# Optimization experiments

Hardware: AMD Instinct MI355X
Metric: run time of the kernel (lower is better)

Reference implementation:

```python
import jax, jax.numpy as jnp
import numpy as np

N_QUBITS = 7
N_LAYERS = 2
HILBERT = 2 ** N_QUBITS


def _rx(t):
    c = jnp.cos(t / 2).astype(jnp.complex64)
    s = (-1j * jnp.sin(t / 2)).astype(jnp.complex64)
    return jnp.stack([jnp.stack([c, s]), jnp.stack([s, c])])


def _ry(t):
    c = jnp.cos(t / 2).astype(jnp.complex64)
    s = jnp.sin(t / 2).astype(jnp.complex64)
    return jnp.stack([jnp.stack([c, -s]), jnp.stack([s, c])])


def _rz(t):
    z0 = jnp.exp(-0.5j * t).astype(jnp.complex64)
    z1 = jnp.exp(0.5j * t).astype(jnp.complex64)
    zero = jnp.zeros_like(z0)
    return jnp.stack([jnp.stack([z0, zero]), jnp.stack([zero, z1])])


def _apply_1q(state, U, q):
    # state: [B, 2, 2, ..., 2]; wire q lives on axis q+1 (wire 0 = MSB, PennyLane convention)
    ax = q + 1
    out = jnp.tensordot(U, state, axes=[[1], [ax]])  # new gate axis at 0
    return jnp.moveaxis(out, 0, ax)


def _apply_cnot(state, c, t):
    c_ax, t_ax = c + 1, t + 1
    s0 = jax.lax.index_in_dim(state, 0, c_ax, keepdims=False)
    s1 = jax.lax.index_in_dim(state, 1, c_ax, keepdims=False)
    t2 = t_ax - 1 if t_ax > c_ax else t_ax  # target axis after control axis removed
    s1 = jnp.flip(s1, axis=t2)  # X on target within control=1 block
    return jnp.stack([s0, s1], axis=c_ax)


def setup_inputs() -> dict:
    key = jax.random.key(0)
    k1, k2 = jax.random.split(key)
    x = jax.random.normal(k1, (131072, HILBERT), dtype=jnp.float32)
    weights = jax.random.uniform(k2, (N_LAYERS, N_QUBITS, 3), dtype=jnp.float32) * (2 * np.pi)
    return {"x": x, "weights": weights}


def reference(x, weights):
    B = x.shape[0]
    norms = jnp.maximum(jnp.linalg.norm(x, axis=-1, keepdims=True), 1e-8)
    psi = (x / norms).astype(jnp.complex64)
    state = psi.reshape((B,) + (2,) * N_QUBITS)
    for layer in range(N_LAYERS):
        for q in range(N_QUBITS):
            state = _apply_1q(state, _rx(weights[layer, q, 0]), q)
            state = _apply_1q(state, _ry(weights[layer, q, 1]), q)
            state = _apply_1q(state, _rz(weights[layer, q, 2]), q)
        for q in range(N_QUBITS):
            state = _apply_cnot(state, q, (q + 1) % N_QUBITS)
    probs = jnp.abs(state) ** 2  # real [B, 2,...,2]
    zs = []
    for q in range(N_QUBITS):
        other = tuple(a for a in range(1, N_QUBITS + 1) if a != q + 1)
        p = probs.sum(axis=other)  # [B, 2] marginal of wire q
        zs.append(p[:, 0] - p[:, 1])
    return jnp.stack(zs, axis=-1)  # [B, N_QUBITS]
```

## Files before the change

kernel.cpp:

```cpp
#include <hip/hip_runtime.h>
#include <hip/hip_bf16.h>


typedef __attribute__((ext_vector_type(8)))  short short8;
typedef __attribute__((ext_vector_type(16))) float f32x16;

static __device__ __forceinline__ short f2bf(float f) {
  __bf16 h = (__bf16)f;
  return __builtin_bit_cast(short, h);
}

static __device__ __forceinline__ int widx(int P, int s, int k) {
  return ((((P << 2) + (s >> 5)) * 8 + (k >> 4)) * 64 +
          ((s & 31) + ((k >> 3) & 1) * 32)) * 8 + (k & 7);
}

__global__ void qnn_build_w(const float* __restrict__ wts,
                            short* __restrict__ W) {
  const int k = blockIdx.x;
  const int l = threadIdx.x;

  float c0r = (2 * l     == k) ? 1.f : 0.f, c0i = 0.f;
  float c1r = (2 * l + 1 == k) ? 1.f : 0.f, c1i = 0.f;

  for (int layer = 0; layer < 2; ++layer) {
    for (int q = 0; q < 7; ++q) {
      const float t0 = 0.5f * wts[(layer * 7 + q) * 3 + 0];
      const float t1 = 0.5f * wts[(layer * 7 + q) * 3 + 1];
      const float t2 = 0.5f * wts[(layer * 7 + q) * 3 + 2];
      const float cx = __cosf(t0), sx = __sinf(t0);
      const float cy = __cosf(t1), sy = __sinf(t1);
      const float cz = __cosf(t2), sz = __sinf(t2);
      const float m00r =  cy * cx, m00i =  sy * sx;
      const float m01r = -sy * cx, m01i = -cy * sx;
      const float m10r =  sy * cx, m10i = -cy * sx;
      const float m11r =  cy * cx, m11i = -sy * sx;
      const float g00r = m00r * cz + m00i * sz, g00i = m00i * cz - m00r * sz;
      const float g01r = m01r * cz + m01i * sz, g01i = m01i * cz - m01r * sz;
      const float g10r = m10r * cz - m10i * sz, g10i = m10i * cz + m10r * sz;
      const float g11r = m11r * cz - m11i * sz, g11i = m11i * cz + m11r * sz;

      const int b = 6 - q;
      if (b == 0) {
        const float n0r = g00r*c0r - g00i*c0i + g01r*c1r - g01i*c1i;
        const float n0i = g00r*c0i + g00i*c0r + g01r*c1i + g01i*c1r;
        const float n1r = g10r*c0r - g10i*c0i + g11r*c1r - g11i*c1i;
        const float n1i = g10r*c0i + g10i*c0r + g11r*c1i + g11i*c1r;
        c0r = n0r; c0i = n0i; c1r = n1r; c1i = n1i;
      } else {
        const int xm  = 1 << (b - 1);
        const int myb = (l >> (b - 1)) & 1;
        const float p0r = __shfl_xor(c0r, xm), p0i = __shfl_xor(c0i, xm);
        const float p1r = __shfl_xor(c1r, xm), p1i = __shfl_xor(c1i, xm);
        const float gar = myb ? g11r : g00r, gai = myb ? g11i : g00i;
        const float gbr = myb ? g10r : g01r, gbi = myb ? g10i : g01i;
        const float n0r = gar*c0r - gai*c0i + gbr*p0r - gbi*p0i;
        const float n0i = gar*c0i + gai*c0r + gbr*p0i + gbi*p0r;
        const float n1r = gar*c1r - gai*c1i + gbr*p1r - gbi*p1i;
        const float n1i = gar*c1i + gai*c1r + gbr*p1i + gbi*p1r;
        c0r = n0r; c0i = n0i; c1r = n1r; c1i = n1i;
      }
    }
    #pragma unroll
    for (int q = 0; q < 7; ++q) {
      const int bc = 6 - q;
      const int bt = 6 - ((q + 1) % 7);
      if (bt == 0) {
        if (l & 1) { float tr=c0r, ti=c0i; c0r=c1r; c0i=c1i; c1r=tr; c1i=ti; }
      } else if (bc == 0) {
        c1r = __shfl_xor(c1r, 32);
        c1i = __shfl_xor(c1i, 32);
      } else {
        const int xm = 1 << (bt - 1);
        const float p0r = __shfl_xor(c0r, xm), p0i = __shfl_xor(c0i, xm);
        const float p1r = __shfl_xor(c1r, xm), p1i = __shfl_xor(c1i, xm);
        if ((l >> (bc - 1)) & 1) { c0r=p0r; c0i=p0i; c1r=p1r; c1i=p1i; }
      }
    }
  }

  W[widx(0, 2 * l,     k)] = f2bf(c0r);
  W[widx(0, 2 * l + 1, k)] = f2bf(c1r);
  W[widx(1, 2 * l,     k)] = f2bf(c0i);
  W[widx(1, 2 * l + 1, k)] = f2bf(c1i);
}

__global__ __launch_bounds__(256, 4) void qnn_main(
    const float* __restrict__ x, const short* __restrict__ W,
    float* __restrict__ out) {
  const int tid = threadIdx.x;
  const int l   = tid & 63;
  const int wv  = tid >> 6;
  const int col = l & 31;
  const int h   = l >> 5;

  __shared__ short8 xb[512];
  __shared__ float  red[4][32][7];

  const int t0 = blockIdx.x;

  float4 fa[2], fb[2];
  #pragma unroll
  for (int i = 0; i < 2; ++i) {
    const int p = i * 256 + tid;
    const int r = p >> 4, q = p & 15;
    const float* gp = x + (size_t)(t0 * 32 + r) * 128 + q * 8;
    fa[i] = *reinterpret_cast<const float4*>(gp);
    fb[i] = *reinterpret_cast<const float4*>(gp + 4);
  }

  short8 A0[8], A1[8];
  #pragma unroll
  for (int j = 0; j < 8; ++j) {
    const int off = ((wv * 8 + j) * 64 + l) * 8;
    A0[j] = *reinterpret_cast<const short8*>(W + off);
    A1[j] = *reinterpret_cast<const short8*>(W + 16384 + off);
  }

  #pragma unroll
  for (int i = 0; i < 2; ++i) {
    const int p = i * 256 + tid;
    const int r = p >> 4, q = p & 15;
    short8 c;
    c[0]=f2bf(fa[i].x); c[1]=f2bf(fa[i].y); c[2]=f2bf(fa[i].z); c[3]=f2bf(fa[i].w);
    c[4]=f2bf(fb[i].x); c[5]=f2bf(fb[i].y); c[6]=f2bf(fb[i].z); c[7]=f2bf(fb[i].w);
    xb[r * 16 + (q ^ (r & 7))] = c;
  }
  asm volatile("s_waitcnt lgkmcnt(0)" ::: "memory");
  __builtin_amdgcn_s_barrier();
  asm volatile("" ::: "memory");

  f32x16 acc0 = {0.f,0.f,0.f,0.f,0.f,0.f,0.f,0.f,
                 0.f,0.f,0.f,0.f,0.f,0.f,0.f,0.f};
  f32x16 acc1 = {0.f,0.f,0.f,0.f,0.f,0.f,0.f,0.f,
                 0.f,0.f,0.f,0.f,0.f,0.f,0.f,0.f};
  #pragma unroll
  for (int j = 0; j < 8; ++j) {
    const int q = j * 2 + h;
    const short8 bfr = xb[col * 16 + (q ^ (col & 7))];
    acc0 = __builtin_amdgcn_mfma_f32_32x32x16_bf16(A0[j], bfr, acc0, 0, 0, 0);
    acc1 = __builtin_amdgcn_mfma_f32_32x32x16_bf16(A1[j], bfr, acc1, 0, 0, 0);
  }

  {
    float aS[8], aD[8];
    #pragma unroll
    for (int i = 0; i < 8; ++i) {
      const float pe = acc0[2*i]   * acc0[2*i]   + acc1[2*i]   * acc1[2*i];
      const float po = acc0[2*i+1] * acc0[2*i+1] + acc1[2*i+1] * acc1[2*i+1];
      aS[i] = pe + po;
      aD[i] = pe - po;
    }
    float bS[4], bD[4];
    #pragma unroll
    for (int i = 0; i < 4; ++i) {
      bS[i] = aS[2*i] + aS[2*i+1];
      bD[i] = aS[2*i] - aS[2*i+1];
    }
    float u0 = ((aD[0]+aD[1]) + (aD[2]+aD[3])) + ((aD[4]+aD[5]) + (aD[6]+aD[7]));
    float u1 = (bD[0] + bD[1]) + (bD[2] + bD[3]);
    const float cS0 = bS[0] + bS[1], cD0 = bS[0] - bS[1];
    const float cS1 = bS[2] + bS[3], cD1 = bS[2] - bS[3];
    float u3 = cD0 + cD1;
    float u4 = cS0 - cS1;
    float T  = cS0 + cS1;

    const float Tp = __shfl_xor(T, 32);
    const float u2 = h ? (Tp - T) : (T - Tp);
    T += Tp;
    u0 += __shfl_xor(u0, 32);
    u1 += __shfl_xor(u1, 32);
    u3 += __shfl_xor(u3, 32);
    u4 += __shfl_xor(u4, 32);

    if (h == 0) {
      red[wv][col][0] = T;
      red[wv][col][1] = u0;
      red[wv][col][2] = u1;
      red[wv][col][3] = u2;
      red[wv][col][4] = u3;
      red[wv][col][5] = u4;
    }
  }

  asm volatile("s_waitcnt lgkmcnt(0)" ::: "memory");
  __builtin_amdgcn_s_barrier();
  asm volatile("" ::: "memory");

  if (tid < 32) {
    const int c = tid;
    const float T0 = red[0][c][0], T1 = red[1][c][0];
    const float T2 = red[2][c][0], T3 = red[3][c][0];
    const float sT  = (T0 + T1) + (T2 + T3);
    const float inv = 1.0f / sT;
    const float z0 = (T0 + T1) - (T2 + T3);
    const float z1 = (T0 - T1) + (T2 - T3);
    float zr[5];
    #pragma unroll
    for (int i = 0; i < 5; ++i)
      zr[i] = (red[0][c][5-i] + red[1][c][5-i]) +
              (red[2][c][5-i] + red[3][c][5-i]);
    float* o = out + (size_t)(t0 * 32 + c) * 7;
    o[0] = z0 * inv; o[1] = z1 * inv; o[2] = zr[0] * inv; o[3] = zr[1] * inv;
    o[4] = zr[2] * inv; o[5] = zr[3] * inv; o[6] = zr[4] * inv;
  }
}

extern "C" void kernel_launch(void* const* d_in, const int* in_sizes, int n_in,
                              void* d_out, int out_size, void* d_ws, size_t ws_size,
                              hipStream_t stream) {
  const float* x   = (const float*)d_in[0];
  const float* wts = (const float*)d_in[1];
  float* out = (float*)d_out;
  short* W   = (short*)d_ws;

  const int B     = in_sizes[0] / 128;
  const int grid  = B / 32;

  qnn_build_w<<<128, 64, 0, stream>>>(wts, W);
  qnn_main<<<grid, 256, 0, stream>>>(x, W, out);
}
```

Before: 25.55 us.

## Make main kernel persistent with double-buffered LDS and prefetched x tiles

Changes the main kernel from one 32-row tile per block to a grid-stride persistent loop over 1024 blocks. The W fragments are loaded into registers once per block. The next tile's x is prefetched into registers and staged into a second LDS buffer while the current tile is computed. This amortises W loads and block launch overhead and overlaps global loads with MFMA work. It adds a loop, doubles the LDS buffers and keeps more registers live, which may reduce occupancy.

```diff
diff --git a/kernel.cpp b/kernel.cpp
--- a/kernel.cpp
+++ b/kernel.cpp
@@ -87,27 +87,15 @@
 
 __global__ __launch_bounds__(256, 4) void qnn_main(
     const float* __restrict__ x, const short* __restrict__ W,
-    float* __restrict__ out) {
+    float* __restrict__ out, int ntiles, int stride) {
   const int tid = threadIdx.x;
   const int l   = tid & 63;
   const int wv  = tid >> 6;
   const int col = l & 31;
   const int h   = l >> 5;
 
-  __shared__ short8 xb[512];
-  __shared__ float  red[4][32][7];
-
-  const int t0 = blockIdx.x;
-
-  float4 fa[2], fb[2];
-  #pragma unroll
-  for (int i = 0; i < 2; ++i) {
-    const int p = i * 256 + tid;
-    const int r = p >> 4, q = p & 15;
-    const float* gp = x + (size_t)(t0 * 32 + r) * 128 + q * 8;
-    fa[i] = *reinterpret_cast<const float4*>(gp);
-    fb[i] = *reinterpret_cast<const float4*>(gp + 4);
-  }
+  __shared__ short8 xb[2][512];
+  __shared__ float  red[2][4][32][6];
 
   short8 A0[8], A1[8];
   #pragma unroll
@@ -117,32 +105,40 @@
     A1[j] = *reinterpret_cast<const short8*>(W + 16384 + off);
   }
 
-  #pragma unroll
-  for (int i = 0; i < 2; ++i) {
-    const int p = i * 256 + tid;
-    const int r = p >> 4, q = p & 15;
-    short8 c;
-    c[0]=f2bf(fa[i].x); c[1]=f2bf(fa[i].y); c[2]=f2bf(fa[i].z); c[3]=f2bf(fa[i].w);
-    c[4]=f2bf(fb[i].x); c[5]=f2bf(fb[i].y); c[6]=f2bf(fb[i].z); c[7]=f2bf(fb[i].w);
-    xb[r * 16 + (q ^ (r & 7))] = c;
-  }
-  asm volatile("s_waitcnt lgkmcnt(0)" ::: "memory");
-  __builtin_amdgcn_s_barrier();
-  asm volatile("" ::: "memory");
-
-  f32x16 acc0 = {0.f,0.f,0.f,0.f,0.f,0.f,0.f,0.f,
-                 0.f,0.f,0.f,0.f,0.f,0.f,0.f,0.f};
-  f32x16 acc1 = {0.f,0.f,0.f,0.f,0.f,0.f,0.f,0.f,
-                 0.f,0.f,0.f,0.f,0.f,0.f,0.f,0.f};
-  #pragma unroll
-  for (int j = 0; j < 8; ++j) {
-    const int q = j * 2 + h;
-    const short8 bfr = xb[col * 16 + (q ^ (col & 7))];
-    acc0 = __builtin_amdgcn_mfma_f32_32x32x16_bf16(A0[j], bfr, acc0, 0, 0, 0);
-    acc1 = __builtin_amdgcn_mfma_f32_32x32x16_bf16(A1[j], bfr, acc1, 0, 0, 0);
-  }
-
-  {
+  float4 fa[2], fb[2];
+  const int r = tid >> 4, q = tid & 15;
+  const int sidx = r * 16 + (q ^ (r & 7));
+  const size_t goff = (size_t)r * 128 + q * 8;
+
+  auto LOAD = [&](int T) {
+    const float* gp = x + (size_t)T * 32 * 128 + goff;
+    fa[0] = *reinterpret_cast<const float4*>(gp);
+    fb[0] = *reinterpret_cast<const float4*>(gp + 4);
+    fa[1] = *reinterpret_cast<const float4*>(gp + 2048);
+    fb[1] = *reinterpret_cast<const float4*>(gp + 2052);
+  };
+  auto STAGE = [&](int b) {
+    #pragma unroll
+    for (int i = 0; i < 2; ++i) {
+      short8 c;
+      c[0]=f2bf(fa[i].x); c[1]=f2bf(fa[i].y); c[2]=f2bf(fa[i].z); c[3]=f2bf(fa[i].w);
+      c[4]=f2bf(fb[i].x); c[5]=f2bf(fb[i].y); c[6]=f2bf(fb[i].z); c[7]=f2bf(fb[i].w);
+      xb[b][sidx + i * 256] = c;
+    }
+  };
+
+  auto COMPUTE = [&](int b) {
+    f32x16 acc0 = {0.f,0.f,0.f,0.f,0.f,0.f,0.f,0.f,
+                   0.f,0.f,0.f,0.f,0.f,0.f,0.f,0.f};
+    f32x16 acc1 = {0.f,0.f,0.f,0.f,0.f,0.f,0.f,0.f,
+                   0.f,0.f,0.f,0.f,0.f,0.f,0.f,0.f};
+    #pragma unroll
+    for (int j = 0; j < 8; ++j) {
+      const int qq = j * 2 + h;
+      const short8 bfr = xb[b][col * 16 + (qq ^ (col & 7))];
+      acc0 = __builtin_amdgcn_mfma_f32_32x32x16_bf16(A0[j], bfr, acc0, 0, 0, 0);
+      acc1 = __builtin_amdgcn_mfma_f32_32x32x16_bf16(A1[j], bfr, acc1, 0, 0, 0);
+    }
     float aS[8], aD[8];
     #pragma unroll
     for (int i = 0; i < 8; ++i) {
@@ -174,35 +170,55 @@
     u4 += __shfl_xor(u4, 32);
 
     if (h == 0) {
-      red[wv][col][0] = T;
-      red[wv][col][1] = u0;
-      red[wv][col][2] = u1;
-      red[wv][col][3] = u2;
-      red[wv][col][4] = u3;
-      red[wv][col][5] = u4;
-    }
-  }
-
+      red[b][wv][col][0] = T;
+      red[b][wv][col][1] = u0;
+      red[b][wv][col][2] = u1;
+      red[b][wv][col][3] = u2;
+      red[b][wv][col][4] = u3;
+      red[b][wv][col][5] = u4;
+    }
+  };
+
+  auto TAIL = [&](int b, int T) {
+    if (tid < 32) {
+      const int c = tid;
+      const float T0v = red[b][0][c][0], T1v = red[b][1][c][0];
+      const float T2v = red[b][2][c][0], T3v = red[b][3][c][0];
+      const float sT  = (T0v + T1v) + (T2v + T3v);
+      const float inv = 1.0f / sT;
+      const float z0 = (T0v + T1v) - (T2v + T3v);
+      const float z1 = (T0v - T1v) + (T2v - T3v);
+      float zr[5];
+      #pragma unroll
+      for (int i = 0; i < 5; ++i)
+        zr[i] = (red[b][0][c][5-i] + red[b][1][c][5-i]) +
+                (red[b][2][c][5-i] + red[b][3][c][5-i]);
+      float* o = out + (size_t)(T * 32 + c) * 7;
+      o[0] = z0 * inv; o[1] = z1 * inv; o[2] = zr[0] * inv; o[3] = zr[1] * inv;
+      o[4] = zr[2] * inv; o[5] = zr[3] * inv; o[6] = zr[4] * inv;
+    }
+  };
+
+  int t = blockIdx.x;
+  LOAD(t);
+  STAGE(0);
+  if (t + stride < ntiles) LOAD(t + stride);
   asm volatile("s_waitcnt lgkmcnt(0)" ::: "memory");
   __builtin_amdgcn_s_barrier();
   asm volatile("" ::: "memory");
 
-  if (tid < 32) {
-    const int c = tid;
-    const float T0 = red[0][c][0], T1 = red[1][c][0];
-    const float T2 = red[2][c][0], T3 = red[3][c][0];
-    const float sT  = (T0 + T1) + (T2 + T3);
-    const float inv = 1.0f / sT;
-    const float z0 = (T0 + T1) - (T2 + T3);
-    const float z1 = (T0 - T1) + (T2 - T3);
-    float zr[5];
-    #pragma unroll
-    for (int i = 0; i < 5; ++i)
-      zr[i] = (red[0][c][5-i] + red[1][c][5-i]) +
-              (red[2][c][5-i] + red[3][c][5-i]);
-    float* o = out + (size_t)(t0 * 32 + c) * 7;
-    o[0] = z0 * inv; o[1] = z1 * inv; o[2] = zr[0] * inv; o[3] = zr[1] * inv;
-    o[4] = zr[2] * inv; o[5] = zr[3] * inv; o[6] = zr[4] * inv;
+  int i = 0;
+  for (; t < ntiles; t += stride, ++i) {
+    const int p = i & 1;
+    COMPUTE(p);
+    if (t + stride < ntiles) {
+      STAGE(p ^ 1);
+      if (t + 2 * stride < ntiles) LOAD(t + 2 * stride);
+    }
+    asm volatile("s_waitcnt lgkmcnt(0)" ::: "memory");
+    __builtin_amdgcn_s_barrier();
+    asm volatile("" ::: "memory");
+    TAIL(p, t);
   }
 }
 
@@ -214,9 +230,10 @@
   float* out = (float*)d_out;
   short* W   = (short*)d_ws;
 
-  const int B     = in_sizes[0] / 128;
-  const int grid  = B / 32;
+  const int B      = in_sizes[0] / 128;
+  const int ntiles = B / 32;
+  const int grid   = ntiles < 1024 ? ntiles : 1024;
 
   qnn_build_w<<<128, 64, 0, stream>>>(wts, W);
-  qnn_main<<<grid, 256, 0, stream>>>(x, W, out);
-}
+  qnn_main<<<grid, 256, 0, stream>>>(x, W, out, ntiles, grid);
+}
```

After: 29.78 us. +16.6%, slower.
